# Kernel tuning notes

Measured on AMD Instinct MI355X. Metric: run time of the kernel, lower is better.

## Reference

```python
import jax, jax.numpy as jnp
import numpy as np

MEMORY_SIZE = 131072
HIDDEN_DIM = 64
EPS = 1e-12  # matches torch.nn.functional.normalize default eps


def _l2_normalize(x):
    # F.normalize: x / max(||x||_2, eps) along last dim
    n = jnp.linalg.norm(x, axis=-1, keepdims=True)
    return x / jnp.maximum(n, EPS)


def setup_inputs() -> dict:
    key = jax.random.key(0)
    k1, k2, k3 = jax.random.split(key, 3)
    memory = jax.random.normal(k1, (MEMORY_SIZE, HIDDEN_DIM), dtype=jnp.float32)
    embeddings = jax.random.normal(k2, (4096, HIDDEN_DIM), dtype=jnp.float32)
    query = jax.random.normal(k3, (2048, HIDDEN_DIM), dtype=jnp.float32)
    return {
        "memory": memory,
        "embeddings": embeddings,
        "query": query,
        "write_ptr": 17,
        "top_k": 10,
    }


def reference(memory, embeddings, query, write_ptr, top_k):
    # ---- update(): circular FIFO scatter write (detached embeddings) ----
    batch_size = embeddings.shape[0]  # 4096 < MEMORY_SIZE -> no index collisions
    pos = (write_ptr + jnp.arange(batch_size)) % MEMORY_SIZE  # [B]
    mem = memory.at[pos].set(jax.lax.stop_gradient(embeddings))

    # ---- query(): cosine-sim scores + topk + gather ----
    query_norm = _l2_normalize(query)            # [Q, D]
    memory_norm = _l2_normalize(mem)             # [N, D]
    scores = query_norm @ memory_norm.T          # [Q, N]
    k = min(top_k, MEMORY_SIZE)
    values, indices = jax.lax.top_k(scores, k)   # [Q, k] each
    retrieved = mem[indices]                     # [Q, k, D]
    return retrieved, values
```

## Files before the change

### kernel.cpp

```cpp
#include <hip/hip_runtime.h>
#include <math.h>

#define DIM    64
#define MAXT   16
#define SLICES 64
#define QB     128
#define CH     16
#define CLCAP  2048
#define NEG_INF (-3.0e38f)
#define MARGIN 0.008f

typedef float f32x4 __attribute__((ext_vector_type(4)));
typedef _Float16 f16x8 __attribute__((ext_vector_type(8)));
typedef unsigned short u16;

__device__ __forceinline__ u16 f2bf(float f) {
  unsigned u = __float_as_uint(f);
  u += 0x7fffu + ((u >> 16) & 1u);
  return (u16)(u >> 16);
}
__device__ __forceinline__ u16 f2h(float f) {
  union { _Float16 h; u16 u; } c; c.h = (_Float16)f; return c.u;
}

__device__ __forceinline__ const float* row_src(int r, const float* __restrict__ mem,
                                                const float* __restrict__ emb,
                                                int wp, int N, int B) {
  int diff = r - wp; if (diff < 0) diff += N;
  return (diff < B) ? (emb + (size_t)diff * DIM) : (mem + (size_t)r * DIM);
}

__device__ __forceinline__ bool rank_below(float a_v, int a_i, float v, int id) {
  return (a_v < v) || (a_v == v && a_i > id);
}

__device__ __forceinline__ void insert_val(float (&lv)[MAXT], float v) {
#pragma unroll
  for (int k = MAXT - 1; k > 0; --k) {
    if (lv[k - 1] < v)      { lv[k] = lv[k - 1]; }
    else if (lv[k] < v)     { lv[k] = v;         }
  }
  if (lv[0] < v) lv[0] = v;
}

__device__ __forceinline__ void insert_pair(float (&lv)[MAXT], int (&li)[MAXT],
                                            float v, int id) {
#pragma unroll
  for (int k = MAXT - 1; k > 0; --k) {
    if (rank_below(lv[k - 1], li[k - 1], v, id)) { lv[k] = lv[k - 1]; li[k] = li[k - 1]; }
    else if (rank_below(lv[k], li[k], v, id))    { lv[k] = v;         li[k] = id;        }
  }
  if (rank_below(lv[0], li[0], v, id)) { lv[0] = v; li[0] = id; }
}

__global__ __launch_bounds__(256)
void prep_kernel(const float* __restrict__ mem, const float* __restrict__ emb,
                 const float* __restrict__ qry, const int* __restrict__ wpp,
                 float* __restrict__ rm, float* __restrict__ rq,
                 u16* __restrict__ Mn, u16* __restrict__ Qn,
                 int N, int B, int Q) {
  const int wp  = *wpp;
  const int row = blockIdx.x * 32 + (threadIdx.x >> 3);
  const int sub = threadIdx.x & 7;
  if (row >= N + Q) return;
  const float* src = (row < N) ? row_src(row, mem, emb, wp, N, B)
                               : (qry + (size_t)(row - N) * DIM);
  const float4* s4 = (const float4*)src + sub * 2;
  float4 a = s4[0], b = s4[1];
  float ss = a.x*a.x + a.y*a.y + a.z*a.z + a.w*a.w
           + b.x*b.x + b.y*b.y + b.z*b.z + b.w*b.w;
  ss += __shfl_xor(ss, 1);
  ss += __shfl_xor(ss, 2);
  ss += __shfl_xor(ss, 4);
  const float inv = 1.0f / fmaxf(sqrtf(ss), 1e-12f);
  uint4 o;
  o.x = (unsigned)f2h(a.x*inv) | ((unsigned)f2h(a.y*inv) << 16);
  o.y = (unsigned)f2h(a.z*inv) | ((unsigned)f2h(a.w*inv) << 16);
  o.z = (unsigned)f2h(b.x*inv) | ((unsigned)f2h(b.y*inv) << 16);
  o.w = (unsigned)f2h(b.z*inv) | ((unsigned)f2h(b.w*inv) << 16);
  u16* dst = (row < N) ? (Mn + (size_t)row * DIM + sub * 8)
                       : (Qn + (size_t)(row - N) * DIM + sub * 8);
  *(uint4*)dst = o;
  if (sub == 0) { if (row < N) rm[row] = inv; else rq[row - N] = inv; }
}

__global__ __launch_bounds__(256, 4)
void chunkmax_kernel(const u16* __restrict__ Mn, const u16* __restrict__ Qn,
                     u16* __restrict__ Cmax, int N, int nch) {
  __shared__ u16 Mb[2][128 * DIM];
  const int tid = threadIdx.x;
  const int w = tid >> 6, l = tid & 63;

  const int id = blockIdx.x + gridDim.x * blockIdx.y;
  const int s  = (id & 7) * 8 + (id >> 7);
  const int qb = (id >> 3) & 15;
  const int q0 = qb * QB;
  const int slice_rows = N / SLICES;
  const int niter = slice_rows / 128;
  const int row_base = s * slice_rows;

  f16x8 qF[2][2];
#pragma unroll
  for (int j = 0; j < 2; ++j)
#pragma unroll
    for (int ks = 0; ks < 2; ++ks)
      qF[j][ks] = *(const f16x8*)(Qn + (size_t)(q0 + (2*w + j)*16 + (l & 15)) * DIM
                                      + ks*32 + (l >> 4)*8);

  const int sblk = (l & 7) ^ (l >> 3);
  const int rbase = (l & 15)*128 + (((l >> 4) ^ (l & 7)) << 4);

  int buf = 0;
  {
    char* lb = (char*)&Mb[0][0] + w*4096;
#pragma unroll
    for (int t = 0; t < 4; ++t) {
      const u16* g = Mn + (size_t)(row_base + w*32 + t*8 + (l >> 3)) * DIM + sblk*8;
      __builtin_amdgcn_global_load_lds((const __attribute__((address_space(1))) unsigned int*)g,
                                       (__attribute__((address_space(3))) unsigned int*)(lb + t*1024), 16, 0, 0);
    }
  }
  __syncthreads();

  for (int c2 = 0; c2 < niter; ++c2) {
    if (c2 + 1 < niter) {
      char* lb = (char*)&Mb[buf ^ 1][0] + w*4096;
      const int rb = row_base + (c2 + 1)*128;
#pragma unroll
      for (int t = 0; t < 4; ++t) {
        const u16* g = Mn + (size_t)(rb + w*32 + t*8 + (l >> 3)) * DIM + sblk*8;
        __builtin_amdgcn_global_load_lds((const __attribute__((address_space(1))) unsigned int*)g,
                                         (__attribute__((address_space(3))) unsigned int*)(lb + t*1024), 16, 0, 0);
      }
    }
    const char* lb = (const char*)&Mb[buf][0];
    float cm[2][8];
#pragma unroll
    for (int t = 0; t < 8; ++t) {
      f16x8 aM0 = *(const f16x8*)(lb + t*2048 + rbase);
      f16x8 aM1 = *(const f16x8*)(lb + t*2048 + (rbase ^ 64));
#pragma unroll
      for (int j = 0; j < 2; ++j) {
        f32x4 acc = {0.f, 0.f, 0.f, 0.f};
        acc = __builtin_amdgcn_mfma_f32_16x16x32_f16(aM0, qF[j][0], acc, 0, 0, 0);
        acc = __builtin_amdgcn_mfma_f32_16x16x32_f16(aM1, qF[j][1], acc, 0, 0, 0);
        float t1 = fmaxf(fmaxf(acc[0], acc[1]), fmaxf(acc[2], acc[3]));
        float t2 = fmaxf(t1, __int_as_float(
                     __builtin_amdgcn_ds_swizzle(__float_as_int(t1), 0x401F)));
        float t3 = fmaxf(t2, __shfl_xor(t2, 32));
        cm[j][t] = t3;
      }
    }
    if (l < 16) {
#pragma unroll
      for (int j = 0; j < 2; ++j) {
        uint4 o;
        o.x = (unsigned)f2bf(cm[j][0]) | ((unsigned)f2bf(cm[j][1]) << 16);
        o.y = (unsigned)f2bf(cm[j][2]) | ((unsigned)f2bf(cm[j][3]) << 16);
        o.z = (unsigned)f2bf(cm[j][4]) | ((unsigned)f2bf(cm[j][5]) << 16);
        o.w = (unsigned)f2bf(cm[j][6]) | ((unsigned)f2bf(cm[j][7]) << 16);
        const int q = q0 + (2*w + j)*16 + l;
        *(uint4*)(Cmax + (size_t)q * nch + s*128 + c2*8) = o;
      }
    }
    __syncthreads();
    buf ^= 1;
  }
}

__global__ __launch_bounds__(256)
void select_kernel(const u16* __restrict__ Cmax, u16* __restrict__ clist,
                   int* __restrict__ ccount, int nch, int K) {
  const int w = threadIdx.x >> 6, l = threadIdx.x & 63;
  const int q = blockIdx.x * 4 + w;
  const u16* row = Cmax + (size_t)q * nch;
  typedef short s16x8 __attribute__((ext_vector_type(8)));

  float lv[MAXT];
#pragma unroll
  for (int k = 0; k < MAXT; ++k) lv[k] = NEG_INF;

#pragma unroll 4
  for (int i = 0; i < 16; ++i) {
    s16x8 x = *(const s16x8*)(row + i*512 + l*8);
#pragma unroll
    for (int e = 0; e < 8; ++e) {
      float v = __uint_as_float(((unsigned)(u16)x[e]) << 16);
      if (v > lv[MAXT - 1]) insert_val(lv, v);
    }
  }

  float mk = NEG_INF;
  for (int r = 0; r < K; ++r) {
    float bv = lv[0]; int bl = l;
#pragma unroll
    for (int it = 0; it < 6; ++it) {
      float ov = __shfl_xor(bv, 1 << it);
      int   ol = __shfl_xor(bl, 1 << it);
      if (ov > bv || (ov == bv && ol < bl)) { bv = ov; bl = ol; }
    }
    mk = bv;
    if (l == bl) {
#pragma unroll
      for (int k = 0; k < MAXT - 1; ++k) lv[k] = lv[k + 1];
      lv[MAXT - 1] = NEG_INF;
    }
  }
  const float tau = mk - MARGIN;

  u16* out = clist + (size_t)q * CLCAP;
  int cnt = 0;
#pragma unroll 4
  for (int i = 0; i < 16; ++i) {
    s16x8 x = *(const s16x8*)(row + i*512 + l*8);
#pragma unroll
    for (int e = 0; e < 8; ++e) {
      const bool p = (__uint_as_float(((unsigned)(u16)x[e]) << 16) >= tau);
      const unsigned long long b = __ballot(p);
      if (p) {
        const int pos = cnt + (int)__popcll(b & ((1ull << l) - 1ull));
        if (pos < CLCAP) out[pos] = (u16)(i*512 + l*8 + e);
      }
      cnt += (int)__popcll(b);
    }
  }
  if (l == 0) ccount[q] = (cnt > CLCAP) ? CLCAP : cnt;
}

__global__ __launch_bounds__(256)
void rescore_kernel(const float* __restrict__ mem, const float* __restrict__ emb,
                    const float* __restrict__ qry, const int* __restrict__ wpp,
                    const float* __restrict__ rm, const float* __restrict__ rq,
                    const u16* __restrict__ clist, const int* __restrict__ ccount,
                    float* __restrict__ out_retr, float* __restrict__ out_vals,
                    int N, int B, int Q, int K) {
  __shared__ float wvS[4 * MAXT];
  __shared__ int   wiS[4 * MAXT];
  __shared__ int   eiS[MAXT];
  const int tid = threadIdx.x;
  const int w = tid >> 6, l = tid & 63;
  const int q = blockIdx.x;
  const int wp = *wpp;

  float4 qv[16];
  {
    const float4* qr4 = (const float4*)(qry + (size_t)q * DIM);
#pragma unroll
    for (int d = 0; d < 16; ++d) qv[d] = qr4[d];
  }
  const float rqv = rq[q];
  const int cnt = ccount[q];
  const u16* cl = clist + (size_t)q * CLCAP;

  float lv[MAXT]; int li[MAXT];
#pragma unroll
  for (int k = 0; k < MAXT; ++k) { lv[k] = NEG_INF; li[k] = 0x7fffffff; }

  for (int i = w*4; i < cnt; i += 16) {
    const int ci_ = i + (l >> 4);
    const bool valid = (ci_ < cnt);
    const int ch = valid ? (int)cl[ci_] : 0;
    const int row = ch * CH + (l & 15);
    const float* mr = row_src(row, mem, emb, wp, N, B);
    float acc = 0.f;
#pragma unroll
    for (int d = 0; d < 16; ++d) {
      float4 m4 = *(const float4*)(mr + d*4);
      float4 q4 = qv[d];
      acc = fmaf(q4.x, m4.x, acc); acc = fmaf(q4.y, m4.y, acc);
      acc = fmaf(q4.z, m4.z, acc); acc = fmaf(q4.w, m4.w, acc);
    }
    const float vv = valid ? acc * rqv * rm[row] : NEG_INF;
    const int  rid = valid ? row : 0x7fffffff;
    if (rank_below(lv[MAXT - 1], li[MAXT - 1], vv, rid)) insert_pair(lv, li, vv, rid);
  }

  for (int r = 0; r < K; ++r) {
    float bv = lv[0]; int bi = li[0];
#pragma unroll
    for (int it = 0; it < 6; ++it) {
      float ov = __shfl_xor(bv, 1 << it);
      int   oi = __shfl_xor(bi, 1 << it);
      if (ov > bv || (ov == bv && oi < bi)) { bv = ov; bi = oi; }
    }
    if (li[0] == bi) {
#pragma unroll
      for (int k = 0; k < MAXT - 1; ++k) { lv[k] = lv[k + 1]; li[k] = li[k + 1]; }
      lv[MAXT - 1] = NEG_INF; li[MAXT - 1] = 0x7fffffff;
    }
    if (l == 0) { wvS[w*MAXT + r] = bv; wiS[w*MAXT + r] = bi; }
  }
  __syncthreads();

  if (w == 0) {
    int hp = 0;
    float hv = NEG_INF; int hi = 0x7fffffff;
    if (l < 4) { hv = wvS[l*MAXT]; hi = wiS[l*MAXT]; }
    for (int r = 0; r < K; ++r) {
      float bv = hv; int bi = hi; int bs = (l < 4) ? l : 0x7fffffff;
#pragma unroll
      for (int it = 0; it < 2; ++it) {
        float ov = __shfl_xor(bv, 1 << it);
        int   oi = __shfl_xor(bi, 1 << it);
        int   os = __shfl_xor(bs, 1 << it);
        if (ov > bv || (ov == bv && oi < bi)) { bv = ov; bi = oi; bs = os; }
      }
      if (l == 0) { out_vals[(size_t)q * K + r] = bv; eiS[r] = bi; }
      if (l < 4 && l == bs) {
        ++hp;
        if (hp < K) { hv = wvS[l*MAXT + hp]; hi = wiS[l*MAXT + hp]; }
        else        { hv = NEG_INF;          hi = 0x7fffffff;       }
      }
    }
  }
  __syncthreads();

  for (int e = tid; e < K * DIM; e += 256) {
    const int kk = e >> 6, d = e & 63;
    const float* mr = row_src(eiS[kk], mem, emb, wp, N, B);
    out_retr[((size_t)q * K + kk) * DIM + d] = mr[d];
  }
}

extern "C" void kernel_launch(void* const* d_in, const int* in_sizes, int n_in,
                              void* d_out, int out_size, void* d_ws, size_t ws_size,
                              hipStream_t stream) {
  const float* mem = (const float*)d_in[0];
  const float* emb = (const float*)d_in[1];
  const float* qry = (const float*)d_in[2];
  const int*   wpp = (const int*)d_in[3];

  const int N = in_sizes[0] / DIM;
  const int B = in_sizes[1] / DIM;
  const int Q = in_sizes[2] / DIM;
  int K = out_size / (Q * (DIM + 1));
  if (K < 1) K = 1;
  if (K > MAXT) K = MAXT;
  const int nch = N / CH;

  float* rm    = (float*)d_ws;
  float* rq    = rm + N;
  u16*   Cmax  = (u16*)(rq + Q);
  u16*   clist = Cmax + (size_t)Q * nch;
  int*   ccount= (int*)(clist + (size_t)Q * CLCAP);
  u16*   Mn    = (u16*)(ccount + Q);
  u16*   Qn    = Mn + (size_t)N * DIM;

  float* out_retr = (float*)d_out;
  float* out_vals = (float*)d_out + (size_t)Q * K * DIM;

  prep_kernel<<<(N + Q) / 32, 256, 0, stream>>>(mem, emb, qry, wpp, rm, rq, Mn, Qn, N, B, Q);

  dim3 g2(Q / QB, SLICES);
  chunkmax_kernel<<<g2, 256, 0, stream>>>(Mn, Qn, Cmax, N, nch);

  select_kernel<<<Q / 4, 256, 0, stream>>>(Cmax, clist, ccount, nch, K);

  rescore_kernel<<<Q, 256, 0, stream>>>(mem, emb, qry, wpp, rm, rq, clist, ccount,
                                        out_retr, out_vals, N, B, Q, K);
}
```

Before: 226.0 us.

## Restructure chunkmax to register-direct loads, fp16 chunk maxima, and LDS-staged rescoring

The chunkmax kernel drops its LDS double buffer. Each wave now loads its own memory rows straight into registers with a register prefetch and runs MFMA against all eight query tiles, writing fp16 chunk maxima instead of bf16. The select kernel converts from fp16, skips 8-element groups whose maximum cannot enter the top list or pass the threshold, and the candidate margin is halved. The rescore kernel stages candidate chunks into swizzled LDS with asynchronous global-to-LDS loads and double buffering, and four lanes now cooperate on each row. The smaller margin and the changed numeric path risk dropping true top-k candidates, and the heavier register use lowers the occupancy bound of chunkmax.

```diff
diff --git a/kernel.cpp b/kernel.cpp
--- a/kernel.cpp
+++ b/kernel.cpp
@@ -8,19 +8,18 @@
 #define CH     16
 #define CLCAP  2048
 #define NEG_INF (-3.0e38f)
-#define MARGIN 0.008f
+#define MARGIN 0.004f
 
 typedef float f32x4 __attribute__((ext_vector_type(4)));
 typedef _Float16 f16x8 __attribute__((ext_vector_type(8)));
+typedef short s16x8 __attribute__((ext_vector_type(8)));
 typedef unsigned short u16;
 
-__device__ __forceinline__ u16 f2bf(float f) {
-  unsigned u = __float_as_uint(f);
-  u += 0x7fffu + ((u >> 16) & 1u);
-  return (u16)(u >> 16);
-}
 __device__ __forceinline__ u16 f2h(float f) {
   union { _Float16 h; u16 u; } c; c.h = (_Float16)f; return c.u;
+}
+__device__ __forceinline__ float h2f(u16 h) {
+  union { u16 u; _Float16 h; } c; c.u = h; return (float)c.h;
 }
 
 __device__ __forceinline__ const float* row_src(int r, const float* __restrict__ mem,
@@ -84,10 +83,9 @@
   if (sub == 0) { if (row < N) rm[row] = inv; else rq[row - N] = inv; }
 }
 
-__global__ __launch_bounds__(256, 4)
+__global__ __launch_bounds__(256, 3)
 void chunkmax_kernel(const u16* __restrict__ Mn, const u16* __restrict__ Qn,
                      u16* __restrict__ Cmax, int N, int nch) {
-  __shared__ u16 Mb[2][128 * DIM];
   const int tid = threadIdx.x;
   const int w = tid >> 6, l = tid & 63;
 
@@ -96,75 +94,61 @@
   const int qb = (id >> 3) & 15;
   const int q0 = qb * QB;
   const int slice_rows = N / SLICES;
-  const int niter = slice_rows / 128;
+  const int nc2 = slice_rows / 128;
   const int row_base = s * slice_rows;
 
-  f16x8 qF[2][2];
-#pragma unroll
-  for (int j = 0; j < 2; ++j)
+  f16x8 qF[8][2];
+#pragma unroll
+  for (int j = 0; j < 8; ++j)
 #pragma unroll
     for (int ks = 0; ks < 2; ++ks)
-      qF[j][ks] = *(const f16x8*)(Qn + (size_t)(q0 + (2*w + j)*16 + (l & 15)) * DIM
+      qF[j][ks] = *(const f16x8*)(Qn + (size_t)(q0 + j*16 + (l & 15)) * DIM
                                       + ks*32 + (l >> 4)*8);
 
-  const int sblk = (l & 7) ^ (l >> 3);
-  const int rbase = (l & 15)*128 + (((l >> 4) ^ (l & 7)) << 4);
-
-  int buf = 0;
-  {
-    char* lb = (char*)&Mb[0][0] + w*4096;
-#pragma unroll
-    for (int t = 0; t < 4; ++t) {
-      const u16* g = Mn + (size_t)(row_base + w*32 + t*8 + (l >> 3)) * DIM + sblk*8;
-      __builtin_amdgcn_global_load_lds((const __attribute__((address_space(1))) unsigned int*)g,
-                                       (__attribute__((address_space(3))) unsigned int*)(lb + t*1024), 16, 0, 0);
-    }
-  }
-  __syncthreads();
-
-  for (int c2 = 0; c2 < niter; ++c2) {
-    if (c2 + 1 < niter) {
-      char* lb = (char*)&Mb[buf ^ 1][0] + w*4096;
-      const int rb = row_base + (c2 + 1)*128;
-#pragma unroll
-      for (int t = 0; t < 4; ++t) {
-        const u16* g = Mn + (size_t)(rb + w*32 + t*8 + (l >> 3)) * DIM + sblk*8;
-        __builtin_amdgcn_global_load_lds((const __attribute__((address_space(1))) unsigned int*)g,
-                                         (__attribute__((address_space(3))) unsigned int*)(lb + t*1024), 16, 0, 0);
+  const size_t lrow = (size_t)(l & 15) * DIM + (l >> 4) * 8;
+  const u16* Abase = Mn + (size_t)(row_base + w * 32) * DIM + lrow;
+
+  f16x8 aC[2][2], aN[2][2];
+#pragma unroll
+  for (int tt = 0; tt < 2; ++tt)
+#pragma unroll
+    for (int ks = 0; ks < 2; ++ks)
+      aC[tt][ks] = *(const f16x8*)(Abase + (size_t)tt*16*DIM + ks*32);
+
+  for (int c2 = 0; c2 < nc2; ++c2) {
+    if (c2 + 1 < nc2) {
+      const u16* nb = Abase + (size_t)(c2 + 1) * 128 * DIM;
+#pragma unroll
+      for (int tt = 0; tt < 2; ++tt)
+#pragma unroll
+        for (int ks = 0; ks < 2; ++ks)
+          aN[tt][ks] = *(const f16x8*)(nb + (size_t)tt*16*DIM + ks*32);
+    }
+#pragma unroll
+    for (int j = 0; j < 8; ++j) {
+      f32x4 a0 = {0.f, 0.f, 0.f, 0.f};
+      f32x4 a1 = {0.f, 0.f, 0.f, 0.f};
+      a0 = __builtin_amdgcn_mfma_f32_16x16x32_f16(aC[0][0], qF[j][0], a0, 0, 0, 0);
+      a0 = __builtin_amdgcn_mfma_f32_16x16x32_f16(aC[0][1], qF[j][1], a0, 0, 0, 0);
+      a1 = __builtin_amdgcn_mfma_f32_16x16x32_f16(aC[1][0], qF[j][0], a1, 0, 0, 0);
+      a1 = __builtin_amdgcn_mfma_f32_16x16x32_f16(aC[1][1], qF[j][1], a1, 0, 0, 0);
+      float m0 = fmaxf(fmaxf(a0[0], a0[1]), fmaxf(a0[2], a0[3]));
+      float m1 = fmaxf(fmaxf(a1[0], a1[1]), fmaxf(a1[2], a1[3]));
+      m0 = fmaxf(m0, __int_as_float(__builtin_amdgcn_ds_swizzle(__float_as_int(m0), 0x401F)));
+      m1 = fmaxf(m1, __int_as_float(__builtin_amdgcn_ds_swizzle(__float_as_int(m1), 0x401F)));
+      m0 = fmaxf(m0, __shfl_xor(m0, 32));
+      m1 = fmaxf(m1, __shfl_xor(m1, 32));
+      if (l < 16) {
+        const int q = q0 + j*16 + l;
+        const unsigned pk = (unsigned)f2h(m0) | ((unsigned)f2h(m1) << 16);
+        *(unsigned*)(Cmax + (size_t)q * nch + s*128 + c2*8 + w*2) = pk;
       }
     }
-    const char* lb = (const char*)&Mb[buf][0];
-    float cm[2][8];
-#pragma unroll
-    for (int t = 0; t < 8; ++t) {
-      f16x8 aM0 = *(const f16x8*)(lb + t*2048 + rbase);
-      f16x8 aM1 = *(const f16x8*)(lb + t*2048 + (rbase ^ 64));
-#pragma unroll
-      for (int j = 0; j < 2; ++j) {
-        f32x4 acc = {0.f, 0.f, 0.f, 0.f};
-        acc = __builtin_amdgcn_mfma_f32_16x16x32_f16(aM0, qF[j][0], acc, 0, 0, 0);
-        acc = __builtin_amdgcn_mfma_f32_16x16x32_f16(aM1, qF[j][1], acc, 0, 0, 0);
-        float t1 = fmaxf(fmaxf(acc[0], acc[1]), fmaxf(acc[2], acc[3]));
-        float t2 = fmaxf(t1, __int_as_float(
-                     __builtin_amdgcn_ds_swizzle(__float_as_int(t1), 0x401F)));
-        float t3 = fmaxf(t2, __shfl_xor(t2, 32));
-        cm[j][t] = t3;
-      }
-    }
-    if (l < 16) {
-#pragma unroll
-      for (int j = 0; j < 2; ++j) {
-        uint4 o;
-        o.x = (unsigned)f2bf(cm[j][0]) | ((unsigned)f2bf(cm[j][1]) << 16);
-        o.y = (unsigned)f2bf(cm[j][2]) | ((unsigned)f2bf(cm[j][3]) << 16);
-        o.z = (unsigned)f2bf(cm[j][4]) | ((unsigned)f2bf(cm[j][5]) << 16);
-        o.w = (unsigned)f2bf(cm[j][6]) | ((unsigned)f2bf(cm[j][7]) << 16);
-        const int q = q0 + (2*w + j)*16 + l;
-        *(uint4*)(Cmax + (size_t)q * nch + s*128 + c2*8) = o;
-      }
-    }
-    __syncthreads();
-    buf ^= 1;
+#pragma unroll
+    for (int tt = 0; tt < 2; ++tt)
+#pragma unroll
+      for (int ks = 0; ks < 2; ++ks)
+        aC[tt][ks] = aN[tt][ks];
   }
 }
 
@@ -174,7 +158,6 @@
   const int w = threadIdx.x >> 6, l = threadIdx.x & 63;
   const int q = blockIdx.x * 4 + w;
   const u16* row = Cmax + (size_t)q * nch;
-  typedef short s16x8 __attribute__((ext_vector_type(8)));
 
   float lv[MAXT];
 #pragma unroll
@@ -183,10 +166,15 @@
 #pragma unroll 4
   for (int i = 0; i < 16; ++i) {
     s16x8 x = *(const s16x8*)(row + i*512 + l*8);
-#pragma unroll
-    for (int e = 0; e < 8; ++e) {
-      float v = __uint_as_float(((unsigned)(u16)x[e]) << 16);
-      if (v > lv[MAXT - 1]) insert_val(lv, v);
+    float v[8];
+#pragma unroll
+    for (int e = 0; e < 8; ++e) v[e] = h2f((u16)x[e]);
+    float mx = fmaxf(fmaxf(fmaxf(v[0], v[1]), fmaxf(v[2], v[3])),
+                     fmaxf(fmaxf(v[4], v[5]), fmaxf(v[6], v[7])));
+    if (mx > lv[MAXT - 1]) {
+#pragma unroll
+      for (int e = 0; e < 8; ++e)
+        if (v[e] > lv[MAXT - 1]) insert_val(lv, v[e]);
     }
   }
 
@@ -213,9 +201,15 @@
 #pragma unroll 4
   for (int i = 0; i < 16; ++i) {
     s16x8 x = *(const s16x8*)(row + i*512 + l*8);
+    float v[8];
+#pragma unroll
+    for (int e = 0; e < 8; ++e) v[e] = h2f((u16)x[e]);
+    float mx = fmaxf(fmaxf(fmaxf(v[0], v[1]), fmaxf(v[2], v[3])),
+                     fmaxf(fmaxf(v[4], v[5]), fmaxf(v[6], v[7])));
+    if (__ballot(mx >= tau) == 0ull) continue;
 #pragma unroll
     for (int e = 0; e < 8; ++e) {
-      const bool p = (__uint_as_float(((unsigned)(u16)x[e]) << 16) >= tau);
+      const bool p = (v[e] >= tau);
       const unsigned long long b = __ballot(p);
       if (p) {
         const int pos = cnt + (int)__popcll(b & ((1ull << l) - 1ull));
@@ -234,6 +228,7 @@
                     const u16* __restrict__ clist, const int* __restrict__ ccount,
                     float* __restrict__ out_retr, float* __restrict__ out_vals,
                     int N, int B, int Q, int K) {
+  __shared__ float chS[4][2][1024];
   __shared__ float wvS[4 * MAXT];
   __shared__ int   wiS[4 * MAXT];
   __shared__ int   eiS[MAXT];
@@ -252,27 +247,50 @@
   const int cnt = ccount[q];
   const u16* cl = clist + (size_t)q * CLCAP;
 
+  const int xd = l & 15;
+
   float lv[MAXT]; int li[MAXT];
 #pragma unroll
   for (int k = 0; k < MAXT; ++k) { lv[k] = NEG_INF; li[k] = 0x7fffffff; }
 
-  for (int i = w*4; i < cnt; i += 16) {
-    const int ci_ = i + (l >> 4);
-    const bool valid = (ci_ < cnt);
-    const int ch = valid ? (int)cl[ci_] : 0;
-    const int row = ch * CH + (l & 15);
-    const float* mr = row_src(row, mem, emb, wp, N, B);
+  const int r4 = l >> 2;
+  const int rsw = r4 & 7;
+  const bool p0 = ((l & 3) == 0);
+
+  int buf = 0;
+  auto issue = [&](int ci, int b) {
+    const int ch = (int)cl[ci];
+#pragma unroll
+    for (int i = 0; i < 4; ++i) {
+      const int rr = i*4 + (l >> 4);
+      const float* rp = row_src(ch * CH + rr, mem, emb, wp, N, B);
+      __builtin_amdgcn_global_load_lds(
+          (const __attribute__((address_space(1))) unsigned int*)(rp + ((xd ^ (rr & 7)) << 2)),
+          (__attribute__((address_space(3))) unsigned int*)&chS[w][b][i * 256], 16, 0, 0);
+    }
+  };
+
+  if (w < cnt) issue(w, 0);
+  for (int ci = w; ci < cnt; ci += 4) {
+    const bool more = (ci + 4 < cnt);
+    if (more) issue(ci + 4, buf ^ 1);
+    if (more) { asm volatile("s_waitcnt vmcnt(4)" ::: "memory"); }
+    else      { asm volatile("s_waitcnt vmcnt(0)" ::: "memory"); }
+    const int ch = (int)cl[ci];
+    const int row = ch * CH + r4;
+    const float* Lr = &chS[w][buf][r4 * 64];
     float acc = 0.f;
 #pragma unroll
-    for (int d = 0; d < 16; ++d) {
-      float4 m4 = *(const float4*)(mr + d*4);
-      float4 q4 = qv[d];
+    for (int d4 = 0; d4 < 16; ++d4) {
+      const float4 m4 = *(const float4*)(Lr + ((d4 ^ rsw) << 2));
+      const float4 q4 = qv[d4];
       acc = fmaf(q4.x, m4.x, acc); acc = fmaf(q4.y, m4.y, acc);
       acc = fmaf(q4.z, m4.z, acc); acc = fmaf(q4.w, m4.w, acc);
     }
-    const float vv = valid ? acc * rqv * rm[row] : NEG_INF;
-    const int  rid = valid ? row : 0x7fffffff;
+    const float vv = p0 ? acc * rqv * rm[row] : NEG_INF;
+    const int  rid = p0 ? row : 0x7fffffff;
     if (rank_below(lv[MAXT - 1], li[MAXT - 1], vv, rid)) insert_pair(lv, li, vv, rid);
+    buf ^= 1;
   }
 
   for (int r = 0; r < K; ++r) {
```

Measured after the change: 262.0 us. 1.16x slower.
